# Kernel tuning notes

Hardware: AMD Instinct MI355X
Metric: run time of the kernel (lower is better)

Reference implementation:

```python
import jax, jax.numpy as jnp
import numpy as np

N_NODES = 50000
N_EDGES = 800000
N_GRAPHS = 64
IN_CH = 128
HID_CH = 128
OUT_CH = 2


def setup_inputs() -> dict:
    key = jax.random.key(0)
    k = jax.random.split(key, 7)
    x = jax.random.normal(k[0], (N_NODES, IN_CH), dtype=jnp.float32)
    edge_index = jax.random.randint(k[1], (2, N_EDGES), 0, N_NODES, dtype=jnp.int64)
    batch = jnp.sort(jax.random.randint(k[2], (N_NODES,), 0, N_GRAPHS, dtype=jnp.int64))
    W1 = jax.random.normal(k[3], (IN_CH, HID_CH), dtype=jnp.float32) * 0.05
    b1 = jnp.zeros((HID_CH,), dtype=jnp.float32)
    W2 = jax.random.normal(k[4], (HID_CH, OUT_CH), dtype=jnp.float32) * 0.05
    b2 = jnp.zeros((OUT_CH,), dtype=jnp.float32)
    return {"x": x, "edge_index": edge_index, "batch": batch,
            "W1": W1, "b1": b1, "W2": W2, "b2": b2}


def gcn_conv(x, edge_index, W, b):
    """PyG GCNConv: add self-loops, symmetric D^{-1/2}(A+I)D^{-1/2} aggregation of XW, plus bias."""
    n = x.shape[0]
    loop = jnp.arange(n, dtype=edge_index.dtype)
    src = jnp.concatenate([edge_index[0], loop])  # [E+N]
    dst = jnp.concatenate([edge_index[1], loop])
    ones = jnp.ones_like(dst, dtype=x.dtype)
    deg = jax.ops.segment_sum(ones, dst, num_segments=n)      # in-degree incl. self-loop (>=1)
    d_inv_sqrt = jax.lax.rsqrt(deg)
    norm = d_inv_sqrt[src] * d_inv_sqrt[dst]                  # [E+N]
    h = x @ W                                                 # [N, out]
    msg = h[src] * norm[:, None]                              # gather + scale
    out = jax.ops.segment_sum(msg, dst, num_segments=n)       # scatter-add
    return out + b


def global_mean_pool(x, batch, num_graphs):
    sums = jax.ops.segment_sum(x, batch, num_segments=num_graphs)
    cnt = jax.ops.segment_sum(jnp.ones((x.shape[0],), dtype=x.dtype), batch, num_segments=num_graphs)
    return sums / jnp.maximum(cnt, 1.0)[:, None]


def reference(x, edge_index, batch, W1, b1, W2, b2):
    h = jax.nn.relu(gcn_conv(x, edge_index, W1, b1))
    h = gcn_conv(h, edge_index, W2, b2)
    out = global_mean_pool(h, batch, N_GRAPHS)  # [G, out_channels]
    # dropout in eval mode == identity
    return out
```

## Files before the change

kernel.cpp:

```cpp
#include <hip/hip_runtime.h>


#define NGRAPH 64
#define CH 128
#define BSUB 384
#define NCOPY 8
#define BCAPT (BSUB * NCOPY)

typedef float f32x4 __attribute__((ext_vector_type(4)));
typedef _Float16 f16x8 __attribute__((ext_vector_type(8)));
typedef _Float16 f16x4 __attribute__((ext_vector_type(4)));
typedef _Float16 f16x2 __attribute__((ext_vector_type(2)));

__global__ void k_init(int* __restrict__ bcur8, int* __restrict__ row_start,
                       float* __restrict__ gsum, int* __restrict__ gcnt,
                       const float* __restrict__ W1, _Float16* __restrict__ w1t,
                       int NB, int N, int E) {
    int i = blockIdx.x * blockDim.x + threadIdx.x;
    if (i < NB * NCOPY) bcur8[i] = 0;
    if (i == 0) row_start[N] = E;
    if (i < 2 * NGRAPH) gsum[i] = 0.f;
    if (i < NGRAPH) gcnt[i] = 0;
    if (i < CH * CH) {
        int k = i >> 7, c = i & 127;
        w1t[c * CH + k] = (_Float16)W1[i];
    }
}

__global__ __launch_bounds__(256) void k_bin(const int* __restrict__ src,
                                             const int* __restrict__ dst,
                                             int* __restrict__ bcur8,
                                             unsigned int* __restrict__ tmp,
                                             int E, int EPB) {
    __shared__ int hist[512];
    __shared__ int gbase[512];
    __shared__ int cur[512];
    int t = threadIdx.x;
    int e0 = blockIdx.x * EPB;
    int e1 = min(E, e0 + EPB);
    for (int i = t; i < 512; i += 256) { hist[i] = 0; cur[i] = 0; }
    __syncthreads();
    for (int e = e0 + t; e < e1; e += 256)
        atomicAdd(&hist[dst[e] >> 7], 1);
    __syncthreads();
    int copy = blockIdx.x & (NCOPY - 1);
    for (int b = t; b < 512; b += 256) {
        int hc = hist[b];
        if (hc) gbase[b] = atomicAdd(&bcur8[b * NCOPY + copy], hc);
    }
    __syncthreads();
    for (int e = e0 + t; e < e1; e += 256) {
        int d = dst[e];
        int b = d >> 7;
        int li = atomicAdd(&cur[b], 1);
        int pos = gbase[b] + li;
        if (pos < BSUB)
            tmp[(size_t)b * BCAPT + copy * BSUB + pos] =
                ((unsigned)(d & 127) << 25) | (unsigned)src[e];
    }
}

__global__ __launch_bounds__(512) void k_bsum(const int* __restrict__ bcur8,
                                              int* __restrict__ bbase, int NB) {
    __shared__ int tmp[512];
    int t = threadIdx.x;
    int v = 0;
    if (t < NB)
        for (int c = 0; c < NCOPY; c++) v += min(bcur8[t * NCOPY + c], BSUB);
    int val = v;
    tmp[t] = val;
    __syncthreads();
    for (int off = 1; off < 512; off <<= 1) {
        int add = (t >= off) ? tmp[t - off] : 0;
        __syncthreads();
        val += add;
        tmp[t] = val;
        __syncthreads();
    }
    if (t < NB) bbase[t] = val - v;
}

__global__ __launch_bounds__(256) void k_build(const unsigned int* __restrict__ tmp,
                                               const int* __restrict__ bcur8,
                                               const int* __restrict__ bbase,
                                               int* __restrict__ row_start,
                                               float* __restrict__ dinv,
                                               int* __restrict__ csr, int N) {
    __shared__ int hist[128];
    __shared__ int scan[128];
    __shared__ int lcur[128];
    int b = blockIdx.x, t = threadIdx.x;
    if (t < 128) hist[t] = 0;
    __syncthreads();
    const unsigned int* tb = tmp + (size_t)b * BCAPT;
    for (int c = 0; c < NCOPY; c++) {
        int cnt = min(bcur8[b * NCOPY + c], BSUB);
        const unsigned int* tp = tb + c * BSUB;
        for (int e = t; e < cnt; e += 256) atomicAdd(&hist[tp[e] >> 25], 1);
    }
    __syncthreads();
    int val = 0, v = 0;
    if (t < 128) { v = hist[t]; val = v; scan[t] = val; }
    __syncthreads();
    for (int off = 1; off < 128; off <<= 1) {
        int add = (t >= off && t < 128) ? scan[t - off] : 0;
        __syncthreads();
        if (t < 128) { val += add; scan[t] = val; }
        __syncthreads();
    }
    int base = bbase[b];
    if (t < 128) {
        int excl = val - v;
        lcur[t] = excl;
        int n = b * 128 + t;
        if (n < N) {
            row_start[n] = base + excl;
            dinv[n] = rsqrtf((float)(v + 1));
        }
    }
    __syncthreads();
    for (int c = 0; c < NCOPY; c++) {
        int cnt = min(bcur8[b * NCOPY + c], BSUB);
        const unsigned int* tp = tb + c * BSUB;
        for (int e = t; e < cnt; e += 256) {
            unsigned p = tp[e];
            int pos = atomicAdd(&lcur[p >> 25], 1);
            csr[base + pos] = (int)(p & 0x01FFFFFFu);
        }
    }
}

__global__ __launch_bounds__(256) void k_gemm1(const float* __restrict__ X,
                                               const _Float16* __restrict__ w1t,
                                               const float* __restrict__ dinv,
                                               _Float16* __restrict__ H, int N) {
    __shared__ _Float16 Xs[64 * 136];
    __shared__ _Float16 Ws[128 * 136];
    int t = threadIdx.x;
    int row0 = blockIdx.x * 64;
    const float4* Xv = (const float4*)X;

    #pragma unroll
    for (int i = 0; i < 8; i++) {
        int gi = t + i * 256;
        int r = gi >> 5, c4 = gi & 31;
        int gr = row0 + r;
        float4 v = (gr < N) ? Xv[(size_t)gr * 32 + c4] : make_float4(0.f, 0.f, 0.f, 0.f);
        f16x4 hv = {(_Float16)v.x, (_Float16)v.y, (_Float16)v.z, (_Float16)v.w};
        *(f16x4*)&Xs[r * 136 + 4 * c4] = hv;
    }
    #pragma unroll
    for (int i = 0; i < 8; i++) {
        int gi = t + i * 256;
        int r = gi >> 4, cc = gi & 15;
        f16x8 vv = *(const f16x8*)&w1t[r * CH + cc * 8];
        *(f16x8*)&Ws[r * 136 + cc * 8] = vv;
    }
    __syncthreads();

    int w = t >> 6, l = t & 63;
    int r0w = w * 16;
    int lr = l & 15, lk = (l >> 4) * 8;
    f32x4 acc[8] = {};
    #pragma unroll
    for (int k0 = 0; k0 < 128; k0 += 32) {
        f16x8 a = *(const f16x8*)&Xs[(r0w + lr) * 136 + k0 + lk];
        #pragma unroll
        for (int c = 0; c < 8; c++) {
            f16x8 bf = *(const f16x8*)&Ws[(c * 16 + lr) * 136 + k0 + lk];
            acc[c] = __builtin_amdgcn_mfma_f32_16x16x32_f16(a, bf, acc[c], 0, 0, 0);
        }
    }
    float dv[4];
    #pragma unroll
    for (int q = 0; q < 4; q++) {
        int gr = row0 + r0w + (l >> 4) * 4 + q;
        dv[q] = (gr < N) ? dinv[gr] : 0.f;
    }
    __syncthreads();
    #pragma unroll
    for (int c = 0; c < 8; c++)
        #pragma unroll
        for (int q = 0; q < 4; q++)
            Xs[(r0w + (l >> 4) * 4 + q) * 136 + c * 16 + lr] = (_Float16)(acc[c][q] * dv[q]);
    __syncthreads();
    f16x2* Hv = (f16x2*)H;
    #pragma unroll
    for (int i = 0; i < 16; i++) {
        int gi = t + i * 256;
        int r = gi >> 6, cp = gi & 63;
        int gr = row0 + r;
        if (gr < N) Hv[(size_t)gr * 64 + cp] = *(f16x2*)&Xs[r * 136 + 2 * cp];
    }
}

__global__ __launch_bounds__(256) void k_layer1(const _Float16* __restrict__ h,
                                                const int* __restrict__ csr,
                                                const int* __restrict__ row_start,
                                                const float* __restrict__ dinv,
                                                const float* __restrict__ b1,
                                                const float* __restrict__ W2,
                                                float* __restrict__ h2, int N) {
    int n = (blockIdx.x * 256 + threadIdx.x) >> 6;
    int l = threadIdx.x & 63;
    if (n >= N) return;
    const f16x2* hv = (const f16x2*)h;
    float dn = dinv[n];
    f16x2 self = hv[(size_t)n * 64 + l];
    float acc0 = (float)self.x, acc1 = (float)self.y;
    int base = row_start[n];
    int cnt = row_start[n + 1] - base;
    for (int c0 = 0; c0 < cnt; c0 += 64) {
        int m = cnt - c0; if (m > 64) m = 64;
        int idx = (c0 + l < cnt) ? csr[base + c0 + l] : 0;
        int j = 0;
        int jm = m & ~7;
        for (; j < jm; j += 8) {
            int s0 = __shfl(idx, j + 0), s1 = __shfl(idx, j + 1);
            int s2 = __shfl(idx, j + 2), s3 = __shfl(idx, j + 3);
            int s4 = __shfl(idx, j + 4), s5 = __shfl(idx, j + 5);
            int s6 = __shfl(idx, j + 6), s7 = __shfl(idx, j + 7);
            f16x2 v0 = hv[(size_t)s0 * 64 + l];
            f16x2 v1 = hv[(size_t)s1 * 64 + l];
            f16x2 v2 = hv[(size_t)s2 * 64 + l];
            f16x2 v3 = hv[(size_t)s3 * 64 + l];
            f16x2 v4 = hv[(size_t)s4 * 64 + l];
            f16x2 v5 = hv[(size_t)s5 * 64 + l];
            f16x2 v6 = hv[(size_t)s6 * 64 + l];
            f16x2 v7 = hv[(size_t)s7 * 64 + l];
            acc0 += (float)v0.x; acc1 += (float)v0.y;
            acc0 += (float)v1.x; acc1 += (float)v1.y;
            acc0 += (float)v2.x; acc1 += (float)v2.y;
            acc0 += (float)v3.x; acc1 += (float)v3.y;
            acc0 += (float)v4.x; acc1 += (float)v4.y;
            acc0 += (float)v5.x; acc1 += (float)v5.y;
            acc0 += (float)v6.x; acc1 += (float)v6.y;
            acc0 += (float)v7.x; acc1 += (float)v7.y;
        }
        for (; j < m; ++j) {
            int s = __shfl(idx, j);
            f16x2 v = hv[(size_t)s * 64 + l];
            acc0 += (float)v.x; acc1 += (float)v.y;
        }
    }
    float2 bb = ((const float2*)b1)[l];
    float v0 = fmaxf(fmaf(dn, acc0, bb.x), 0.f);
    float v1 = fmaxf(fmaf(dn, acc1, bb.y), 0.f);
    float4 w2 = ((const float4*)W2)[l];
    float p0 = fmaf(v0, w2.x, v1 * w2.z);
    float p1 = fmaf(v0, w2.y, v1 * w2.w);
    #pragma unroll
    for (int off = 32; off; off >>= 1) {
        p0 += __shfl_xor(p0, off);
        p1 += __shfl_xor(p1, off);
    }
    if (l == 0) ((float2*)h2)[n] = make_float2(p0 * dn, p1 * dn);
}

__global__ __launch_bounds__(256) void k_layer2_pool(const float* __restrict__ h2,
                                                     const int* __restrict__ csr,
                                                     const int* __restrict__ row_start,
                                                     const float* __restrict__ dinv,
                                                     const int* __restrict__ batch,
                                                     float* __restrict__ gsum,
                                                     int* __restrict__ gcnt, int N) {
    __shared__ float ssum[2 * NGRAPH];
    __shared__ int scnt[NGRAPH];
    int t = threadIdx.x;
    if (t < 2 * NGRAPH) ssum[t] = 0.f;
    if (t < NGRAPH) scnt[t] = 0;
    __syncthreads();
    int n = blockIdx.x * blockDim.x + t;
    if (n < N) {
        const float2* h2v = (const float2*)h2;
        float dn = dinv[n];
        float2 a = h2v[n];
        int base = row_start[n], end = row_start[n + 1];
        for (int e = base; e < end; e++) {
            float2 v = h2v[csr[e]];
            a.x += v.x;
            a.y += v.y;
        }
        a.x *= dn;
        a.y *= dn;
        int g = batch[n];
        atomicAdd(&ssum[g * 2 + 0], a.x);
        atomicAdd(&ssum[g * 2 + 1], a.y);
        atomicAdd(&scnt[g], 1);
    }
    __syncthreads();
    if (t < 2 * NGRAPH) atomicAdd(&gsum[t], ssum[t]);
    if (t < NGRAPH) atomicAdd(&gcnt[t], scnt[t]);
}

__global__ void k_final(const float* __restrict__ gsum, const int* __restrict__ gcnt,
                        const float* __restrict__ b2, float* __restrict__ out) {
    int t = threadIdx.x;
    if (t < 2 * NGRAPH) {
        int g = t >> 1, c = t & 1;
        float cnt = fmaxf((float)gcnt[g], 1.f);
        out[t] = gsum[t] / cnt + b2[c];
    }
}

extern "C" void kernel_launch(void* const* d_in, const int* in_sizes, int n_in,
                              void* d_out, int out_size, void* d_ws, size_t ws_size,
                              hipStream_t stream) {
    const float* x     = (const float*)d_in[0];
    const int*   ei    = (const int*)d_in[1];
    const int*   batch = (const int*)d_in[2];
    const float* W1    = (const float*)d_in[3];
    const float* b1    = (const float*)d_in[4];
    const float* W2    = (const float*)d_in[5];
    const float* b2    = (const float*)d_in[6];
    float* out = (float*)d_out;

    int N = in_sizes[0] / CH;
    int E = in_sizes[1] / 2;
    int NB = (N + 127) / 128;
    const int* esrc = ei;
    const int* edst = ei + E;

    char* w = (char*)d_ws;
    auto alloc = [&](size_t bytes) -> void* {
        void* p = (void*)w;
        w += (bytes + 255) & ~(size_t)255;
        return p;
    };
    _Float16* h      = (_Float16*)alloc((size_t)N * CH * sizeof(_Float16));
    float* dinv      = (float*)alloc((size_t)N * sizeof(float));
    int* row_start   = (int*)  alloc((size_t)(N + 1) * sizeof(int));
    int* csr         = (int*)  alloc((size_t)E * sizeof(int));
    float* h2        = (float*)alloc((size_t)N * 2 * sizeof(float));
    int* bcur8       = (int*)  alloc((size_t)NB * NCOPY * sizeof(int));
    int* bbase       = (int*)  alloc((size_t)NB * sizeof(int));
    _Float16* w1t    = (_Float16*)alloc((size_t)CH * CH * sizeof(_Float16));
    float* gsum      = (float*)alloc(128 * sizeof(float));
    int* gcnt        = (int*)  alloc(64 * sizeof(int));
    unsigned int* tmp = (unsigned int*)h;

    int nbN = (N + 255) / 256;
    int NCHUNK = 256;
    int EPB = (E + NCHUNK - 1) / NCHUNK;

    k_init  <<<64, 256, 0, stream>>>(bcur8, row_start, gsum, gcnt, W1, w1t, NB, N, E);
    k_bin   <<<NCHUNK, 256, 0, stream>>>(esrc, edst, bcur8, tmp, E, EPB);
    k_bsum  <<<1, 512, 0, stream>>>(bcur8, bbase, NB);
    k_build <<<NB, 256, 0, stream>>>(tmp, bcur8, bbase, row_start, dinv, csr, N);
    k_gemm1 <<<(N + 63) / 64, 256, 0, stream>>>(x, w1t, dinv, h, N);
    k_layer1<<<(N * 64 + 255) / 256, 256, 0, stream>>>(h, csr, row_start, dinv, b1, W2, h2, N);
    k_layer2_pool<<<nbN, 256, 0, stream>>>(h2, csr, row_start, dinv, batch, gsum, gcnt, N);
    k_final <<<1, 128, 0, stream>>>(gsum, gcnt, b2, out);
}
```

Before: 174.9 us.

## Use fixed-stride padded CSR buckets and fold final pooling into layer2

Replaces the global prefix-scan over buckets with a fixed per-bucket stride in the CSR, which removes the k_bsum launch. Each row's neighbour list is padded to a multiple of 8 with a dummy index N that points at a zero row, so the layer1 gather loop has no remainder tail. The final mean-pool division moves into the last block of k_layer2_pool through a done counter, removing the k_final launch. The costs are extra padded-edge traffic, including the padding loop in layer2, and a fixed capacity assumption that a bucket holds no more than 4096 edges.

Result: faster. 169.7 us (-3.0%).

```diff
diff --git a/kernel.cpp b/kernel.cpp
--- a/kernel.cpp
+++ b/kernel.cpp
@@ -6,21 +6,24 @@
 #define BSUB 384
 #define NCOPY 8
 #define BCAPT (BSUB * NCOPY)
+#define CSTR 4096
 
 typedef float f32x4 __attribute__((ext_vector_type(4)));
 typedef _Float16 f16x8 __attribute__((ext_vector_type(8)));
 typedef _Float16 f16x4 __attribute__((ext_vector_type(4)));
 typedef _Float16 f16x2 __attribute__((ext_vector_type(2)));
 
-__global__ void k_init(int* __restrict__ bcur8, int* __restrict__ row_start,
-                       float* __restrict__ gsum, int* __restrict__ gcnt,
+__global__ void k_init(int* __restrict__ bcur8, float* __restrict__ gsum,
+                       int* __restrict__ gcnt, int* __restrict__ done,
+                       float* __restrict__ h2,
                        const float* __restrict__ W1, _Float16* __restrict__ w1t,
-                       int NB, int N, int E) {
+                       int NB, int N) {
     int i = blockIdx.x * blockDim.x + threadIdx.x;
     if (i < NB * NCOPY) bcur8[i] = 0;
-    if (i == 0) row_start[N] = E;
     if (i < 2 * NGRAPH) gsum[i] = 0.f;
     if (i < NGRAPH) gcnt[i] = 0;
+    if (i == 0) *done = 0;
+    if (i < 2) h2[2 * N + i] = 0.f;
     if (i < CH * CH) {
         int k = i >> 7, c = i & 127;
         w1t[c * CH + k] = (_Float16)W1[i];
@@ -60,30 +63,9 @@
     }
 }
 
-__global__ __launch_bounds__(512) void k_bsum(const int* __restrict__ bcur8,
-                                              int* __restrict__ bbase, int NB) {
-    __shared__ int tmp[512];
-    int t = threadIdx.x;
-    int v = 0;
-    if (t < NB)
-        for (int c = 0; c < NCOPY; c++) v += min(bcur8[t * NCOPY + c], BSUB);
-    int val = v;
-    tmp[t] = val;
-    __syncthreads();
-    for (int off = 1; off < 512; off <<= 1) {
-        int add = (t >= off) ? tmp[t - off] : 0;
-        __syncthreads();
-        val += add;
-        tmp[t] = val;
-        __syncthreads();
-    }
-    if (t < NB) bbase[t] = val - v;
-}
-
 __global__ __launch_bounds__(256) void k_build(const unsigned int* __restrict__ tmp,
                                                const int* __restrict__ bcur8,
-                                               const int* __restrict__ bbase,
-                                               int* __restrict__ row_start,
+                                               int2* __restrict__ rs2,
                                                float* __restrict__ dinv,
                                                int* __restrict__ csr, int N) {
     __shared__ int hist[128];
@@ -99,8 +81,8 @@
         for (int e = t; e < cnt; e += 256) atomicAdd(&hist[tp[e] >> 25], 1);
     }
     __syncthreads();
-    int val = 0, v = 0;
-    if (t < 128) { v = hist[t]; val = v; scan[t] = val; }
+    int val = 0, v = 0, pv = 0;
+    if (t < 128) { v = hist[t]; pv = (v + 7) & ~7; val = pv; scan[t] = val; }
     __syncthreads();
     for (int off = 1; off < 128; off <<= 1) {
         int add = (t >= off && t < 128) ? scan[t - off] : 0;
@@ -108,14 +90,15 @@
         if (t < 128) { val += add; scan[t] = val; }
         __syncthreads();
     }
-    int base = bbase[b];
+    int base = b * CSTR;
     if (t < 128) {
-        int excl = val - v;
+        int excl = val - pv;
         lcur[t] = excl;
         int n = b * 128 + t;
         if (n < N) {
-            row_start[n] = base + excl;
+            rs2[n] = make_int2(base + excl, pv);
             dinv[n] = rsqrtf((float)(v + 1));
+            for (int e = v; e < pv; e++) csr[base + excl + e] = N;
         }
     }
     __syncthreads();
@@ -190,13 +173,13 @@
         int gi = t + i * 256;
         int r = gi >> 6, cp = gi & 63;
         int gr = row0 + r;
-        if (gr < N) Hv[(size_t)gr * 64 + cp] = *(f16x2*)&Xs[r * 136 + 2 * cp];
+        Hv[(size_t)gr * 64 + cp] = *(f16x2*)&Xs[r * 136 + 2 * cp];
     }
 }
 
 __global__ __launch_bounds__(256) void k_layer1(const _Float16* __restrict__ h,
                                                 const int* __restrict__ csr,
-                                                const int* __restrict__ row_start,
+                                                const int2* __restrict__ rs2,
                                                 const float* __restrict__ dinv,
                                                 const float* __restrict__ b1,
                                                 const float* __restrict__ W2,
@@ -208,14 +191,12 @@
     float dn = dinv[n];
     f16x2 self = hv[(size_t)n * 64 + l];
     float acc0 = (float)self.x, acc1 = (float)self.y;
-    int base = row_start[n];
-    int cnt = row_start[n + 1] - base;
+    int2 rs = rs2[n];
+    int base = rs.x, cnt = rs.y;
     for (int c0 = 0; c0 < cnt; c0 += 64) {
         int m = cnt - c0; if (m > 64) m = 64;
-        int idx = (c0 + l < cnt) ? csr[base + c0 + l] : 0;
-        int j = 0;
-        int jm = m & ~7;
-        for (; j < jm; j += 8) {
+        int idx = csr[base + c0 + l];
+        for (int j = 0; j < m; j += 8) {
             int s0 = __shfl(idx, j + 0), s1 = __shfl(idx, j + 1);
             int s2 = __shfl(idx, j + 2), s3 = __shfl(idx, j + 3);
             int s4 = __shfl(idx, j + 4), s5 = __shfl(idx, j + 5);
@@ -237,11 +218,6 @@
             acc0 += (float)v6.x; acc1 += (float)v6.y;
             acc0 += (float)v7.x; acc1 += (float)v7.y;
         }
-        for (; j < m; ++j) {
-            int s = __shfl(idx, j);
-            f16x2 v = hv[(size_t)s * 64 + l];
-            acc0 += (float)v.x; acc1 += (float)v.y;
-        }
     }
     float2 bb = ((const float2*)b1)[l];
     float v0 = fmaxf(fmaf(dn, acc0, bb.x), 0.f);
@@ -259,13 +235,17 @@
 
 __global__ __launch_bounds__(256) void k_layer2_pool(const float* __restrict__ h2,
                                                      const int* __restrict__ csr,
-                                                     const int* __restrict__ row_start,
+                                                     const int2* __restrict__ rs2,
                                                      const float* __restrict__ dinv,
                                                      const int* __restrict__ batch,
                                                      float* __restrict__ gsum,
-                                                     int* __restrict__ gcnt, int N) {
+                                                     int* __restrict__ gcnt,
+                                                     int* __restrict__ done,
+                                                     const float* __restrict__ b2,
+                                                     float* __restrict__ out, int N) {
     __shared__ float ssum[2 * NGRAPH];
     __shared__ int scnt[NGRAPH];
+    __shared__ int s_last;
     int t = threadIdx.x;
     if (t < 2 * NGRAPH) ssum[t] = 0.f;
     if (t < NGRAPH) scnt[t] = 0;
@@ -275,8 +255,8 @@
         const float2* h2v = (const float2*)h2;
         float dn = dinv[n];
         float2 a = h2v[n];
-        int base = row_start[n], end = row_start[n + 1];
-        for (int e = base; e < end; e++) {
+        int2 rs = rs2[n];
+        for (int e = rs.x; e < rs.x + rs.y; e++) {
             float2 v = h2v[csr[e]];
             a.x += v.x;
             a.y += v.y;
@@ -291,15 +271,18 @@
     __syncthreads();
     if (t < 2 * NGRAPH) atomicAdd(&gsum[t], ssum[t]);
     if (t < NGRAPH) atomicAdd(&gcnt[t], scnt[t]);
-}
-
-__global__ void k_final(const float* __restrict__ gsum, const int* __restrict__ gcnt,
-                        const float* __restrict__ b2, float* __restrict__ out) {
-    int t = threadIdx.x;
-    if (t < 2 * NGRAPH) {
+    __syncthreads();
+    if (t == 0) {
+        __threadfence();
+        int r = atomicAdd(done, 1);
+        s_last = (r == (int)gridDim.x - 1) ? 1 : 0;
+    }
+    __syncthreads();
+    if (s_last && t < 2 * NGRAPH) {
         int g = t >> 1, c = t & 1;
-        float cnt = fmaxf((float)gcnt[g], 1.f);
-        out[t] = gsum[t] / cnt + b2[c];
+        float sv = atomicAdd(&gsum[t], 0.f);
+        float cv = (float)atomicAdd(&gcnt[g], 0);
+        out[t] = sv / fmaxf(cv, 1.f) + b2[c];
     }
 }
 
@@ -327,28 +310,27 @@
         w += (bytes + 255) & ~(size_t)255;
         return p;
     };
-    _Float16* h      = (_Float16*)alloc((size_t)N * CH * sizeof(_Float16));
+    _Float16* h      = (_Float16*)alloc((size_t)(N + 64) * CH * sizeof(_Float16));
     float* dinv      = (float*)alloc((size_t)N * sizeof(float));
-    int* row_start   = (int*)  alloc((size_t)(N + 1) * sizeof(int));
-    int* csr         = (int*)  alloc((size_t)E * sizeof(int));
-    float* h2        = (float*)alloc((size_t)N * 2 * sizeof(float));
+    int2* rs2        = (int2*) alloc((size_t)N * sizeof(int2));
+    int* csr         = (int*)  alloc((size_t)NB * CSTR * sizeof(int));
+    float* h2        = (float*)alloc((size_t)(N + 1) * 2 * sizeof(float));
     int* bcur8       = (int*)  alloc((size_t)NB * NCOPY * sizeof(int));
-    int* bbase       = (int*)  alloc((size_t)NB * sizeof(int));
     _Float16* w1t    = (_Float16*)alloc((size_t)CH * CH * sizeof(_Float16));
     float* gsum      = (float*)alloc(128 * sizeof(float));
     int* gcnt        = (int*)  alloc(64 * sizeof(int));
+    int* done        = (int*)  alloc(256);
     unsigned int* tmp = (unsigned int*)h;
 
     int nbN = (N + 255) / 256;
     int NCHUNK = 256;
     int EPB = (E + NCHUNK - 1) / NCHUNK;
 
-    k_init  <<<64, 256, 0, stream>>>(bcur8, row_start, gsum, gcnt, W1, w1t, NB, N, E);
+    k_init  <<<64, 256, 0, stream>>>(bcur8, gsum, gcnt, done, h2, W1, w1t, NB, N);
     k_bin   <<<NCHUNK, 256, 0, stream>>>(esrc, edst, bcur8, tmp, E, EPB);
-    k_bsum  <<<1, 512, 0, stream>>>(bcur8, bbase, NB);
-    k_build <<<NB, 256, 0, stream>>>(tmp, bcur8, bbase, row_start, dinv, csr, N);
+    k_build <<<NB, 256, 0, stream>>>(tmp, bcur8, rs2, dinv, csr, N);
     k_gemm1 <<<(N + 63) / 64, 256, 0, stream>>>(x, w1t, dinv, h, N);
-    k_layer1<<<(N * 64 + 255) / 256, 256, 0, stream>>>(h, csr, row_start, dinv, b1, W2, h2, N);
-    k_layer2_pool<<<nbN, 256, 0, stream>>>(h2, csr, row_start, dinv, batch, gsum, gcnt, N);
-    k_final <<<1, 128, 0, stream>>>(gsum, gcnt, b2, out);
-}
+    k_layer1<<<(N * 64 + 255) / 256, 256, 0, stream>>>(h, csr, rs2, dinv, b1, W2, h2, N);
+    k_layer2_pool<<<nbN, 256, 0, stream>>>(h2, csr, rs2, dinv, batch, gsum, gcnt,
+                                           done, b2, out, N);
+}
```
